# Performance work log

Measured on AMD Instinct MI355X. Metric: run time of the kernel, lower is better.

Reference implementation:

```python
import jax, jax.numpy as jnp
import numpy as np

EPS = 1e-8
NU_MOLECULAR = 1.5e-05
# loss weights (module defaults)
DATA_W, BC_W, TURB_W, RANS_W, SMOOTH_W, WALL_W = 1.0, 0.05, 0.05, 0.05, 0.01, 0.02
CONT_INIT = CONT_TGT = 0.1
MOM_INIT = MOM_TGT = 0.1
RAMP_STEPS, RAMP_START = 1000, 0

N_NODES, N_EDGES = 100000, 6400000


def _curriculum_weights(step):
    if step < RAMP_START:
        return CONT_INIT, MOM_INIT
    if step >= RAMP_START + RAMP_STEPS:
        return CONT_TGT, MOM_TGT
    alpha = (step - RAMP_START) / RAMP_STEPS  # linear ramp
    return ((1 - alpha) * CONT_INIT + alpha * CONT_TGT,
            (1 - alpha) * MOM_INIT + alpha * MOM_TGT)


def setup_inputs() -> dict:
    key = jax.random.key(0)
    k1, k2, k3, k4, k5 = jax.random.split(key, 5)
    predictions = jax.random.normal(k1, (N_NODES, 4), dtype=jnp.float32)
    targets = jax.random.normal(k2, (N_NODES, 4), dtype=jnp.float32)
    # dx, dy strictly positive edge offsets
    edge_attr_dxdy = jax.random.uniform(k3, (N_EDGES, 2), dtype=jnp.float32, minval=1e-3, maxval=0.05)
    edge_index = jax.random.randint(k4, (2, N_EDGES), 0, N_NODES, dtype=jnp.int64)
    wall_mask = jax.random.bernoulli(k5, 0.05, (N_NODES,))
    return {"predictions": predictions, "targets": targets,
            "edge_attr_dxdy": edge_attr_dxdy, "edge_index": edge_index,
            "wall_mask": wall_mask, "step": 500}


def reference(predictions, targets, edge_attr_dxdy, edge_index, wall_mask, step):
    cont_w, mom_w = _curriculum_weights(int(step))
    N = predictions.shape[0]
    row, col = edge_index[0], edge_index[1]
    u, v, p, nu_t = (predictions[:, i] for i in range(4))
    dx, dy = edge_attr_dxdy[:, 0], edge_attr_dxdy[:, 1]

    # per-edge finite differences (single gather of node fields)
    du = u[col] - u[row]
    dv = v[col] - v[row]
    dp = p[col] - p[row]

    seg = lambda e: jax.ops.segment_sum(e, row, num_segments=N)
    edge_count = jnp.maximum(seg(jnp.ones_like(du)), 1.0)

    # --- data loss ---
    mse_loss = jnp.mean((predictions - targets) ** 2)

    # --- continuity (divergence) loss ---
    divergence = (seg(du / (dx + EPS)) + seg(dv / (dy + EPS))) / edge_count
    div_loss = jnp.mean(divergence ** 2)

    # --- momentum loss ---
    p_grad_x = seg(dp / (dx + EPS)) / edge_count
    p_grad_y = seg(dp / (dy + EPS)) / edge_count
    lap_u = seg(du / (dx ** 2 + EPS)) / edge_count
    lap_v = seg(dv / (dy ** 2 + EPS)) / edge_count
    nu_eff = NU_MOLECULAR + nu_t
    momentum_loss = jnp.mean((p_grad_x + nu_eff * lap_u) ** 2 +
                             (p_grad_y + nu_eff * lap_v) ** 2)

    # --- turbulence losses ---
    positivity_loss = jnp.mean(jax.nn.relu(-nu_t) ** 2)
    du_dx = du / (dx + EPS)
    du_dy = du / (dy + EPS)
    dv_dx = dv / (dx + EPS)
    dv_dy = dv / (dy + EPS)
    strain_sq_edge = 2.0 * (du_dx ** 2 + dv_dy ** 2) + (du_dy + dv_dx) ** 2
    strain_node = seg(strain_sq_edge) / edge_count
    production = nu_t * strain_node
    turb_production_loss = jnp.mean(production ** 2)
    turb_dissipation_loss = jnp.mean(nu_t ** 2)

    # --- boundary-condition & wall-function losses (wall mask) ---
    m = wall_mask.astype(u.dtype)
    n_wall = jnp.maximum(jnp.sum(m), 1.0)
    bc_loss = jnp.sum(m * (u ** 2 + v ** 2)) / n_wall
    wall_loss = jnp.sum(m * (u ** 2 + v ** 2 + nu_t ** 2)) / n_wall

    # --- smoothness loss over edges ---
    smooth_loss = jnp.mean((predictions[col] - predictions[row]) ** 2)

    total = (DATA_W * mse_loss + cont_w * div_loss + mom_w * momentum_loss +
             TURB_W * turb_production_loss + RANS_W * turb_dissipation_loss +
             BC_W * bc_loss + SMOOTH_W * smooth_loss + WALL_W * wall_loss)
    # positivity_loss is tracked but not weighted into total (per visible code paths)
    return total
```

## Files before the change

kernel.cpp:

```cpp
#include <hip/hip_runtime.h>
#include <hip/hip_fp16.h>

#define EPS 1e-8f
#define NU_MOL 1.5e-5f
#define NPB 512
#define MAXNB 256
#define NBP 256
#define NBLK 4096
#define CMAX 1664
#define KMAX 7
#define CH 2048
#define SPLIT 6
#define NGRP 64
#define GRP 64


union U32H2 { unsigned u; __half2 h; };

__device__ inline unsigned packh2(float a, float b) {
    U32H2 x; x.h = __halves2half2(__float2half_rn(a), __float2half_rn(b));
    return x.u;
}
__device__ inline float2 unpackh2(unsigned u) {
    U32H2 x; x.u = u;
    return make_float2(__low2float(x.h), __high2float(x.h));
}
__device__ inline unsigned bf16rne(float f) {
    unsigned u = __float_as_uint(f);
    u += 0x7FFFu + ((u >> 16) & 1u);
    return u >> 16;
}
__device__ inline float bf16dec(unsigned h) {
    return __uint_as_float(h << 16);
}

__device__ inline int detect64(const void* eidx, int N) {
    const long long* ll = (const long long*)eidx;
    int is64 = 1;
    #pragma unroll
    for (int i = 0; i < 16; ++i) {
        long long v = ll[i];
        if (v < 0 || v >= (long long)N) is64 = 0;
    }
    return is64;
}


__global__ void detect_idx_dtype(const void* eidx, int N, int* flag) {
    const long long* ll = (const long long*)eidx;
    int is64 = 1;
    for (int i = 0; i < 16; ++i) {
        long long v = ll[i];
        if (v < 0 || v >= (long long)N) { is64 = 0; break; }
    }
    *flag = is64;
}

__global__ void finalize_kernel(const double* __restrict__ d,
                                const double* __restrict__ smooth_slots,
                                int N, int E, float* __restrict__ out)
{
    double smooth = 0.0;
    for (int i = 0; i < 64; ++i) smooth += smooth_slots[i];
    double dN = (double)N;
    double n_wall = d[5] > 1.0 ? d[5] : 1.0;
    double total = 1.0  * d[0] / (4.0 * dN)
                 + 0.1  * d[1] / dN
                 + 0.1  * d[2] / dN
                 + 0.05 * d[3] / dN
                 + 0.05 * d[4] / dN
                 + 0.05 * d[6] / n_wall
                 + 0.01 * smooth / (4.0 * (double)E)
                 + 0.02 * d[7] / n_wall;
    out[0] = (float)total;
}


__global__ __launch_bounds__(256) void count_kernel(
    const void* __restrict__ eidx, int E, int N, int NB,
    unsigned* __restrict__ counts)
{
    __shared__ unsigned hist[2][MAXNB];
    hist[0][threadIdx.x] = 0u;
    hist[1][threadIdx.x] = 0u;
    __syncthreads();
    const int w = (threadIdx.x >> 6) & 1;
    const int is64 = detect64(eidx, N);
    const long long* ll = (const long long*)eidx;
    const int* ii = (const int*)eidx;
    int chunk = (E + NBLK - 1) / NBLK;
    int s = blockIdx.x * chunk;
    int Cb = min(chunk, E - s);

    unsigned rr[KMAX];
    #pragma unroll
    for (int k = 0; k < KMAX; ++k) {
        int i = k * 256 + threadIdx.x;
        if (i < Cb) {
            int r = is64 ? (int)ll[s + i] : ii[s + i];
            rr[k] = (unsigned)min(max(r, 0), N - 1);
        } else rr[k] = 0xFFFFFFFFu;
    }
    #pragma unroll
    for (int k = 0; k < KMAX; ++k)
        if (rr[k] != 0xFFFFFFFFu)
            atomicAdd(&hist[w][rr[k] >> 9], 1u);
    __syncthreads();
    if (threadIdx.x < NB)
        counts[(size_t)blockIdx.x * NBP + threadIdx.x] =
            hist[0][threadIdx.x] + hist[1][threadIdx.x];
}

__global__ __launch_bounds__(256) void group_sums_kernel(
    const unsigned* __restrict__ counts, unsigned* __restrict__ gsum, int NB)
{
    __shared__ unsigned red[4][64];
    int g = blockIdx.x;
    int b0 = blockIdx.y * 64;
    int j = threadIdx.x & 63, seg = threadIdx.x >> 6;
    int b = b0 + j;
    unsigned ssum = 0;
    if (b < NB) {
        #pragma unroll
        for (int k = 0; k < 16; ++k) {
            int row = g * GRP + seg * 16 + k;
            ssum += counts[(size_t)row * NBP + b];
        }
    }
    red[seg][j] = ssum;
    __syncthreads();
    if (seg == 0 && b < NB)
        gsum[(size_t)g * NBP + b] = red[0][j] + red[1][j] + red[2][j] + red[3][j];
}

__global__ __launch_bounds__(512) void scan_base_kernel(
    unsigned* __restrict__ gsum, unsigned* __restrict__ base, int NB)
{
    __shared__ unsigned sc[512];
    int t = threadIdx.x;
    unsigned vg[NGRP];
    unsigned total = 0;
    if (t < NB) {
        #pragma unroll
        for (int g = 0; g < NGRP; ++g) {
            vg[g] = gsum[(size_t)g * NBP + t];
            total += vg[g];
        }
    }
    sc[t] = total; __syncthreads();
    for (int off = 1; off < 512; off <<= 1) {
        unsigned x = (t >= off) ? sc[t - off] : 0u;
        __syncthreads();
        sc[t] += x;
        __syncthreads();
    }
    unsigned ex = sc[t] - total;
    if (t < NB) {
        base[t] = ex;
        unsigned run = ex;
        #pragma unroll
        for (int g = 0; g < NGRP; ++g) {
            unsigned x = vg[g];
            gsum[(size_t)g * NBP + t] = run;
            run += x;
        }
    }
    if (t == 511) base[NB] = sc[511];
}

__global__ __launch_bounds__(256) void local_scan_kernel(
    unsigned* __restrict__ counts, const unsigned* __restrict__ gsum, int NB)
{
    __shared__ unsigned segs[4][64];
    int g = blockIdx.x;
    int b0 = blockIdx.y * 64;
    int j = threadIdx.x & 63, seg = threadIdx.x >> 6;
    int b = b0 + j;
    unsigned v[16];
    unsigned ssum = 0;
    if (b < NB) {
        #pragma unroll
        for (int k = 0; k < 16; ++k) {
            int row = g * GRP + seg * 16 + k;
            v[k] = counts[(size_t)row * NBP + b];
            ssum += v[k];
        }
    }
    segs[seg][j] = ssum;
    __syncthreads();
    if (b < NB) {
        unsigned carry = gsum[(size_t)g * NBP + b];
        for (int s_ = 0; s_ < seg; ++s_) carry += segs[s_][j];
        #pragma unroll
        for (int k = 0; k < 16; ++k) {
            int row = g * GRP + seg * 16 + k;
            counts[(size_t)row * NBP + b] = carry;
            carry += v[k];
        }
    }
}

__global__ __launch_bounds__(256) void scatter_kernel(
    const void* __restrict__ eidx, const float2* __restrict__ eattr,
    int E, int N, int NB,
    const unsigned* __restrict__ localoff ,
    uint2* __restrict__ vals)
{
    __shared__ unsigned hist[2][MAXNB];
    __shared__ unsigned cur[MAXNB];
    __shared__ unsigned gb2[MAXNB];
    __shared__ uint2 pl[CMAX];
    __shared__ unsigned char bb[CMAX];
    __shared__ unsigned wt[4];

    const int t = threadIdx.x;
    const int blk = blockIdx.x;
    const int lane = t & 63, wv = t >> 6;
    const int w = wv & 1;
    const int is64 = detect64(eidx, N);
    const long long* ll = (const long long*)eidx;
    const int* ii = (const int*)eidx;
    const int chunk = (E + NBLK - 1) / NBLK;
    const int s = blk * chunk;
    const int Cb = min(chunk, E - s);

    hist[0][t] = 0u;
    hist[1][t] = 0u;
    __syncthreads();

    unsigned rr[KMAX], rk[KMAX];
    #pragma unroll
    for (int k = 0; k < KMAX; ++k) {
        int i = k * 256 + t;
        if (i < Cb) {
            int r = is64 ? (int)ll[s + i] : ii[s + i];
            rr[k] = (unsigned)min(max(r, 0), N - 1);
        } else rr[k] = 0xFFFFFFFFu;
    }
    #pragma unroll
    for (int k = 0; k < KMAX; ++k)
        if (rr[k] != 0xFFFFFFFFu)
            rk[k] = atomicAdd(&hist[w][rr[k] >> 9], 1u);
    if (t < NB) gb2[t] = localoff[(size_t)blk * NBP + t];
    __syncthreads();

    unsigned h = hist[0][t] + hist[1][t];
    unsigned x = h;
    #pragma unroll
    for (int off = 1; off < 64; off <<= 1) {
        unsigned y = (unsigned)__shfl_up((int)x, off, 64);
        if (lane >= off) x += y;
    }
    if (lane == 63) wt[wv] = x;
    __syncthreads();
    unsigned wadd = 0;
    for (int w2 = 0; w2 < wv; ++w2) wadd += wt[w2];
    unsigned ex = x + wadd - h;
    cur[t] = ex;
    __syncthreads();
    if (t < NB) gb2[t] -= cur[t];

    int cc[KMAX]; float2 dd[KMAX];
    #pragma unroll
    for (int k = 0; k < KMAX; ++k) {
        int i = k * 256 + t;
        if (i < Cb) {
            int e = s + i;
            cc[k] = is64 ? (int)ll[(long long)E + e] : ii[E + e];
            dd[k] = eattr[e];
        }
    }
    #pragma unroll
    for (int k = 0; k < KMAX; ++k) {
        int i = k * 256 + t;
        if (i < Cb) {
            unsigned r = rr[k];
            unsigned b = r >> 9;
            unsigned rl = r & (NPB - 1);
            int c = min(max(cc[k], 0), N - 1);
            unsigned slot = cur[b] + (w ? hist[0][b] : 0u) + rk[k];
            pl[slot] = make_uint2((unsigned)c | (rl << 17),
                                  packh2(dd[k].x, dd[k].y));
            bb[slot] = (unsigned char)b;
        }
    }
    __syncthreads();

    uint2 op[KMAX]; unsigned ob[KMAX];
    #pragma unroll
    for (int k = 0; k < KMAX; ++k) {
        int p = k * 256 + t;
        if (p < Cb) { op[k] = pl[p]; ob[k] = (unsigned)bb[p]; }
    }
    #pragma unroll
    for (int k = 0; k < KMAX; ++k) {
        int p = k * 256 + t;
        if (p < Cb) vals[gb2[ob[k]] + (unsigned)p] = op[k];
    }
}

__global__ __launch_bounds__(512) void accum_kernel(
    const uint2* __restrict__ vals, const unsigned* __restrict__ base,
    const float4* __restrict__ pred, int N,
    float* __restrict__ g , double* __restrict__ smooth_slots)
{
    __shared__ uint2 pl[CH];
    __shared__ uint2 ph[NPB];
    __shared__ unsigned hist[NPB];
    __shared__ unsigned cur[NPB];
    __shared__ unsigned wt[8];
    __shared__ double sm[8];

    const int b = blockIdx.x;
    const int t = threadIdx.x;
    const int wv = t >> 6, lane = t & 63;
    const int n0 = b * NPB;

    {
        int n = n0 + t;
        float4 p = (n < N) ? pred[n] : make_float4(0.f, 0.f, 0.f, 0.f);
        ph[t] = make_uint2(packh2(p.x, p.y), packh2(p.z, p.w));
    }

    unsigned s0 = base[b], e0 = base[b + 1];
    unsigned len = e0 - s0;
    unsigned s = s0 + (unsigned)(((unsigned long long)len * blockIdx.y) / SPLIT);
    unsigned e = s0 + (unsigned)(((unsigned long long)len * (blockIdx.y + 1)) / SPLIT);

    float cnt = 0, sdiv = 0, smx = 0, smy = 0, sstr = 0;
    double smooth = 0.0;

    for (unsigned cs = s; cs < e; cs += CH) {
        const int n = (int)min((unsigned)CH, e - cs);
        hist[t] = 0u;
        __syncthreads();

        uint2 vv[4]; unsigned rk2[4]; float4 pcc[4];
        #pragma unroll
        for (int k = 0; k < 4; ++k) {
            int i = k * 512 + t;
            if (i < n) vv[k] = vals[cs + i];
            else vv[k].x = 0xFFFFFFFFu;
        }
        #pragma unroll
        for (int k = 0; k < 4; ++k) {
            int i = k * 512 + t;
            if (i < n) {
                rk2[k] = atomicAdd(&hist[(vv[k].x >> 17) & (NPB - 1)], 1u);
                pcc[k] = pred[vv[k].x & 0x1FFFFu];
            }
        }
        __syncthreads();

        unsigned v = hist[t];
        unsigned x = v;
        #pragma unroll
        for (int off = 1; off < 64; off <<= 1) {
            unsigned y = (unsigned)__shfl_up((int)x, off, 64);
            if (lane >= off) x += y;
        }
        if (lane == 63) wt[wv] = x;
        __syncthreads();
        unsigned wadd = 0;
        for (int w = 0; w < wv; ++w) wadd += wt[w];
        unsigned incl = x + wadd;
        unsigned ex0 = incl - v;
        cur[t] = ex0;
        cnt += (float)v;
        __syncthreads();

        #pragma unroll
        for (int k = 0; k < 4; ++k) {
            int i = k * 512 + t;
            if (i >= n) continue;
            unsigned pk = vv[k].x;
            unsigned rl = (pk >> 17) & (NPB - 1);
            float2 dxy = unpackh2(vv[k].y);
            float4 pc = pcc[k];
            uint2 pru = ph[rl];
            float2 pxy = unpackh2(pru.x);
            float2 pzw = unpackh2(pru.y);
            float du = pc.x - pxy.x, dv = pc.y - pxy.y;
            float dp = pc.z - pzw.x, dn = pc.w - pzw.y;
            float rx  = 1.0f / (dxy.x + EPS);
            float ry  = 1.0f / (dxy.y + EPS);
            float rx2 = 1.0f / (dxy.x * dxy.x + EPS);
            float ry2 = 1.0f / (dxy.y * dxy.y + EPS);
            float du_dx = du * rx, du_dy = du * ry;
            float dv_dx = dv * rx, dv_dy = dv * ry;
            float nu_eff = NU_MOL + pzw.y;
            float sh = du_dy + dv_dx;
            float div_e = du_dx + dv_dy;
            float mx_e  = dp * rx + nu_eff * du * rx2;
            float my_e  = dp * ry + nu_eff * dv * ry2;
            float str_e = 2.0f * (du_dx * du_dx + dv_dy * dv_dy) + sh * sh;
            unsigned pos = cur[rl] + rk2[k];
            pl[pos] = make_uint2(bf16rne(div_e) | (bf16rne(mx_e) << 16),
                                 bf16rne(my_e) | (bf16rne(str_e) << 16));
            smooth += (double)(du * du + dv * dv + dp * dp + dn * dn);
        }
        __syncthreads();

        for (unsigned i = ex0; i < incl; ++i) {
            uint2 pv = pl[i];
            sdiv += bf16dec(pv.x & 0xFFFFu);
            smx  += bf16dec(pv.x >> 16);
            smy  += bf16dec(pv.y & 0xFFFFu);
            sstr += bf16dec(pv.y >> 16);
        }
        __syncthreads();
    }

    {
        int n = n0 + t;
        if (n < N) {
            atomicAdd(&g[0 * (size_t)N + n], cnt);
            atomicAdd(&g[1 * (size_t)N + n], sdiv);
            atomicAdd(&g[2 * (size_t)N + n], smx);
            atomicAdd(&g[3 * (size_t)N + n], smy);
            atomicAdd(&g[4 * (size_t)N + n], sstr);
        }
    }

    for (int off = 32; off > 0; off >>= 1)
        smooth += __shfl_down(smooth, off);
    if (lane == 0) sm[wv] = smooth;
    __syncthreads();
    if (t == 0) {
        double tot = 0;
        #pragma unroll
        for (int w = 0; w < 8; ++w) tot += sm[w];
        atomicAdd(&smooth_slots[(b * SPLIT + blockIdx.y) & 63], tot);
    }
}

__global__ __launch_bounds__(256) void node_final_kernel(
    const float* __restrict__ g, const float4* __restrict__ pred,
    const float4* __restrict__ tgt, const unsigned char* __restrict__ wall,
    int N, double* __restrict__ d)
{
    int i = blockIdx.x * 256 + threadIdx.x;
    double v0 = 0, v1 = 0, v2 = 0, v3 = 0, v4 = 0, v5 = 0, v6 = 0, v7 = 0;
    if (i < N) {
        float cnt = g[0 * (size_t)N + i];
        float inv = 1.0f / fmaxf(cnt, 1.0f);
        float div = g[1 * (size_t)N + i] * inv;
        float mx  = g[2 * (size_t)N + i] * inv;
        float my  = g[3 * (size_t)N + i] * inv;
        float sn  = g[4 * (size_t)N + i] * inv;
        float4 p = pred[i];
        float4 tg = tgt[i];
        float prod = p.w * sn;
        float m = wall[i] ? 1.0f : 0.0f;
        float e0 = p.x - tg.x, e1 = p.y - tg.y, e2 = p.z - tg.z, e3 = p.w - tg.w;
        float uv = p.x * p.x + p.y * p.y;
        v0 = (double)(e0 * e0 + e1 * e1 + e2 * e2 + e3 * e3);
        v1 = (double)div * (double)div;
        v2 = (double)mx * (double)mx + (double)my * (double)my;
        v3 = (double)prod * (double)prod;
        v4 = (double)p.w * (double)p.w;
        v5 = (double)m;
        v6 = (double)(m * uv);
        v7 = (double)(m * (uv + p.w * p.w));
    }
    for (int off = 32; off > 0; off >>= 1) {
        v0 += __shfl_down(v0, off); v1 += __shfl_down(v1, off);
        v2 += __shfl_down(v2, off); v3 += __shfl_down(v3, off);
        v4 += __shfl_down(v4, off); v5 += __shfl_down(v5, off);
        v6 += __shfl_down(v6, off); v7 += __shfl_down(v7, off);
    }
    __shared__ double sm[4][8];
    int lane = threadIdx.x & 63, wv = threadIdx.x >> 6;
    if (lane == 0) {
        sm[wv][0] = v0; sm[wv][1] = v1; sm[wv][2] = v2; sm[wv][3] = v3;
        sm[wv][4] = v4; sm[wv][5] = v5; sm[wv][6] = v6; sm[wv][7] = v7;
    }
    __syncthreads();
    if (threadIdx.x < 8) {
        int q = threadIdx.x;
        atomicAdd(&d[q], sm[0][q] + sm[1][q] + sm[2][q] + sm[3][q]);
    }
}


__global__ __launch_bounds__(256) void edge_kernel(
    const void* __restrict__ eidx, const float2* __restrict__ eattr,
    const float4* __restrict__ pred, int E, int N, const int* __restrict__ flag,
    float* __restrict__ a_cnt, float* __restrict__ a_div,
    float* __restrict__ a_mx, float* __restrict__ a_my,
    float* __restrict__ a_str, double* __restrict__ smooth_slots)
{
    const int is64 = *flag;
    const long long* ll = (const long long*)eidx;
    const int* ii = (const int*)eidx;
    double smooth = 0.0;
    const int stride = gridDim.x * blockDim.x;
    for (int e = blockIdx.x * blockDim.x + threadIdx.x; e < E; e += stride) {
        int row, col;
        if (is64) { row = (int)ll[e]; col = (int)ll[(long long)E + e]; }
        else      { row = ii[e];      col = ii[E + e]; }
        row = min(max(row, 0), N - 1);
        col = min(max(col, 0), N - 1);
        float2 dxy = eattr[e];
        float4 pr = pred[row];
        float4 pc = pred[col];
        float du = pc.x - pr.x, dv = pc.y - pr.y;
        float dp = pc.z - pr.z, dn = pc.w - pr.w;
        float rx  = 1.0f / (dxy.x + EPS);
        float ry  = 1.0f / (dxy.y + EPS);
        float rx2 = 1.0f / (dxy.x * dxy.x + EPS);
        float ry2 = 1.0f / (dxy.y * dxy.y + EPS);
        float du_dx = du * rx, du_dy = du * ry;
        float dv_dx = dv * rx, dv_dy = dv * ry;
        float nu_eff = NU_MOL + pr.w;
        atomicAdd(&a_cnt[row], 1.0f);
        atomicAdd(&a_div[row], du_dx + dv_dy);
        atomicAdd(&a_mx[row], dp * rx + nu_eff * du * rx2);
        atomicAdd(&a_my[row], dp * ry + nu_eff * dv * ry2);
        float sh = du_dy + dv_dx;
        atomicAdd(&a_str[row], 2.0f * (du_dx * du_dx + dv_dy * dv_dy) + sh * sh);
        smooth += (double)(du * du + dv * dv + dp * dp + dn * dn);
    }
    for (int off = 32; off > 0; off >>= 1)
        smooth += __shfl_down(smooth, off);
    __shared__ double sm[4];
    int lane = threadIdx.x & 63, wv = threadIdx.x >> 6;
    if (lane == 0) sm[wv] = smooth;
    __syncthreads();
    if (threadIdx.x == 0)
        atomicAdd(&smooth_slots[blockIdx.x & 63], sm[0] + sm[1] + sm[2] + sm[3]);
}

__global__ __launch_bounds__(256) void node_kernel(
    const float4* __restrict__ pred, const float4* __restrict__ tgt,
    const unsigned char* __restrict__ wall, int N,
    const float* __restrict__ a_cnt, const float* __restrict__ a_div,
    const float* __restrict__ a_mx, const float* __restrict__ a_my,
    const float* __restrict__ a_str, double* __restrict__ d)
{
    int i = blockIdx.x * blockDim.x + threadIdx.x;
    double v0 = 0, v1 = 0, v2 = 0, v3 = 0, v4 = 0, v5 = 0, v6 = 0, v7 = 0;
    if (i < N) {
        float4 p = pred[i];
        float4 t = tgt[i];
        float inv = 1.0f / fmaxf(a_cnt[i], 1.0f);
        float div = a_div[i] * inv;
        float mx = a_mx[i] * inv, my = a_my[i] * inv;
        float sn = a_str[i] * inv;
        float prod = p.w * sn;
        float m = wall[i] ? 1.0f : 0.0f;
        float e0 = p.x - t.x, e1 = p.y - t.y, e2 = p.z - t.z, e3 = p.w - t.w;
        float uv = p.x * p.x + p.y * p.y;
        v0 = (double)(e0 * e0 + e1 * e1 + e2 * e2 + e3 * e3);
        v1 = (double)div * (double)div;
        v2 = (double)mx * (double)mx + (double)my * (double)my;
        v3 = (double)prod * (double)prod;
        v4 = (double)p.w * (double)p.w;
        v5 = (double)m;
        v6 = (double)(m * uv);
        v7 = (double)(m * (uv + p.w * p.w));
    }
    for (int off = 32; off > 0; off >>= 1) {
        v0 += __shfl_down(v0, off); v1 += __shfl_down(v1, off);
        v2 += __shfl_down(v2, off); v3 += __shfl_down(v3, off);
        v4 += __shfl_down(v4, off); v5 += __shfl_down(v5, off);
        v6 += __shfl_down(v6, off); v7 += __shfl_down(v7, off);
    }
    __shared__ double sm[4][8];
    int lane = threadIdx.x & 63, wv = threadIdx.x >> 6;
    if (lane == 0) {
        sm[wv][0] = v0; sm[wv][1] = v1; sm[wv][2] = v2; sm[wv][3] = v3;
        sm[wv][4] = v4; sm[wv][5] = v5; sm[wv][6] = v6; sm[wv][7] = v7;
    }
    __syncthreads();
    if (threadIdx.x < 8) {
        int q = threadIdx.x;
        atomicAdd(&d[q], sm[0][q] + sm[1][q] + sm[2][q] + sm[3][q]);
    }
}


extern "C" void kernel_launch(void* const* d_in, const int* in_sizes, int n_in,
                              void* d_out, int out_size, void* d_ws, size_t ws_size,
                              hipStream_t stream) {
    const float4* pred = (const float4*)d_in[0];
    const float4* tgt  = (const float4*)d_in[1];
    const float2* eattr = (const float2*)d_in[2];
    const void* eidx = d_in[3];
    const unsigned char* wall = (const unsigned char*)d_in[4];
    int N = in_sizes[0] / 4;
    int E = in_sizes[2] / 2;
    int NB = (N + NPB - 1) / NPB;
    int chunk = (E + NBLK - 1) / NBLK;
    int ntiles = (NB + 63) / 64;

    char* ws = (char*)d_ws;
    double* d = (double*)ws;
    double* smooth_slots = d + 8;
    int* flag = (int*)(ws + 576);

    size_t off = 1024;
    float* g        = (float*)(ws + off);     off += (size_t)5 * N * 4;
    unsigned* counts = (unsigned*)(ws + off); off += (size_t)NBLK * NBP * 4;
    unsigned* gsum   = (unsigned*)(ws + off); off += (size_t)NGRP * NBP * 4;
    unsigned* base   = (unsigned*)(ws + off); off += (size_t)(NB + 1) * 4;
    off = (off + 15) & ~(size_t)15;
    uint2* vals      = (uint2*)(ws + off);    off += (size_t)E * 8;
    size_t need_fast = off;

    bool fast = (NB <= MAXNB) && (N <= 131072) && (chunk <= CMAX) &&
                (ws_size >= need_fast);

    if (fast) {
        hipMemsetAsync(d_ws, 0, 1024 + (size_t)5 * N * 4, stream);
        count_kernel<<<NBLK, 256, 0, stream>>>(eidx, E, N, NB, counts);
        group_sums_kernel<<<dim3(NGRP, ntiles), 256, 0, stream>>>(counts, gsum, NB);
        scan_base_kernel<<<1, 512, 0, stream>>>(gsum, base, NB);
        local_scan_kernel<<<dim3(NGRP, ntiles), 256, 0, stream>>>(counts, gsum, NB);
        scatter_kernel<<<NBLK, 256, 0, stream>>>(eidx, eattr, E, N, NB,
                                                 counts, vals);
        accum_kernel<<<dim3(NB, SPLIT), 512, 0, stream>>>(vals, base, pred, N,
                                                          g, smooth_slots);
        node_final_kernel<<<(N + 255) / 256, 256, 0, stream>>>(g, pred, tgt, wall,
                                                               N, d);
        finalize_kernel<<<1, 1, 0, stream>>>(d, smooth_slots, N, E, (float*)d_out);
    } else {
        float* arrays = (float*)(ws + 1024);
        float* a_cnt = arrays + (size_t)0 * N;
        float* a_div = arrays + (size_t)1 * N;
        float* a_mx  = arrays + (size_t)2 * N;
        float* a_my  = arrays + (size_t)3 * N;
        float* a_str = arrays + (size_t)4 * N;
        size_t zbytes = 1024 + (size_t)5 * N * sizeof(float);
        hipMemsetAsync(d_ws, 0, zbytes, stream);
        detect_idx_dtype<<<1, 1, 0, stream>>>(eidx, N, flag);
        edge_kernel<<<4096, 256, 0, stream>>>(eidx, eattr, pred, E, N, flag,
                                              a_cnt, a_div, a_mx, a_my, a_str,
                                              smooth_slots);
        node_kernel<<<(N + 255) / 256, 256, 0, stream>>>(pred, tgt, wall, N,
                                                         a_cnt, a_div, a_mx, a_my,
                                                         a_str, d);
        finalize_kernel<<<1, 1, 0, stream>>>(d, smooth_slots, N, E, (float*)d_out);
    }
}
```

Before: 236.7 us.

## Replace per-block scan hierarchy with atomic cursors and LDS float atomics in accumulation

The three-kernel two-level prefix scan over per-block bucket counts is replaced by a global atomic histogram, a single small scan kernel, and atomic cursor reservation inside the scatter kernel. The accumulation kernel drops its local counting sort and bf16 staging buffer. It now accumulates the five per-node sums with shared-memory float atomics and keeps predictions in fp32 in LDS. This removes several launches, the large counts array traffic and many barriers. In exchange it adds LDS atomic contention on hot row slots and makes the edge ordering within buckets nondeterministic.

```diff
diff --git a/kernel.cpp b/kernel.cpp
--- a/kernel.cpp
+++ b/kernel.cpp
@@ -5,14 +5,10 @@
 #define NU_MOL 1.5e-5f
 #define NPB 512
 #define MAXNB 256
-#define NBP 256
 #define NBLK 4096
 #define CMAX 1664
 #define KMAX 7
-#define CH 2048
 #define SPLIT 6
-#define NGRP 64
-#define GRP 64
 
 
 union U32H2 { unsigned u; __half2 h; };
@@ -24,14 +20,6 @@
 __device__ inline float2 unpackh2(unsigned u) {
     U32H2 x; x.u = u;
     return make_float2(__low2float(x.h), __high2float(x.h));
-}
-__device__ inline unsigned bf16rne(float f) {
-    unsigned u = __float_as_uint(f);
-    u += 0x7FFFu + ((u >> 16) & 1u);
-    return u >> 16;
-}
-__device__ inline float bf16dec(unsigned h) {
-    return __uint_as_float(h << 16);
 }
 
 __device__ inline int detect64(const void* eidx, int N) {
@@ -78,7 +66,7 @@
 
 __global__ __launch_bounds__(256) void count_kernel(
     const void* __restrict__ eidx, int E, int N, int NB,
-    unsigned* __restrict__ counts)
+    unsigned* __restrict__ tot)
 {
     __shared__ unsigned hist[2][MAXNB];
     hist[0][threadIdx.x] = 0u;
@@ -106,104 +94,40 @@
         if (rr[k] != 0xFFFFFFFFu)
             atomicAdd(&hist[w][rr[k] >> 9], 1u);
     __syncthreads();
-    if (threadIdx.x < NB)
-        counts[(size_t)blockIdx.x * NBP + threadIdx.x] =
-            hist[0][threadIdx.x] + hist[1][threadIdx.x];
-}
-
-__global__ __launch_bounds__(256) void group_sums_kernel(
-    const unsigned* __restrict__ counts, unsigned* __restrict__ gsum, int NB)
-{
-    __shared__ unsigned red[4][64];
-    int g = blockIdx.x;
-    int b0 = blockIdx.y * 64;
-    int j = threadIdx.x & 63, seg = threadIdx.x >> 6;
-    int b = b0 + j;
-    unsigned ssum = 0;
-    if (b < NB) {
-        #pragma unroll
-        for (int k = 0; k < 16; ++k) {
-            int row = g * GRP + seg * 16 + k;
-            ssum += counts[(size_t)row * NBP + b];
-        }
-    }
-    red[seg][j] = ssum;
-    __syncthreads();
-    if (seg == 0 && b < NB)
-        gsum[(size_t)g * NBP + b] = red[0][j] + red[1][j] + red[2][j] + red[3][j];
-}
-
-__global__ __launch_bounds__(512) void scan_base_kernel(
-    unsigned* __restrict__ gsum, unsigned* __restrict__ base, int NB)
-{
-    __shared__ unsigned sc[512];
+    if (threadIdx.x < NB) {
+        unsigned h = hist[0][threadIdx.x] + hist[1][threadIdx.x];
+        if (h) atomicAdd(&tot[threadIdx.x], h);
+    }
+}
+
+__global__ __launch_bounds__(256) void scan_small_kernel(
+    const unsigned* __restrict__ tot, unsigned* __restrict__ base,
+    unsigned* __restrict__ cursor, int NB)
+{
+    __shared__ unsigned wt[4];
     int t = threadIdx.x;
-    unsigned vg[NGRP];
-    unsigned total = 0;
-    if (t < NB) {
-        #pragma unroll
-        for (int g = 0; g < NGRP; ++g) {
-            vg[g] = gsum[(size_t)g * NBP + t];
-            total += vg[g];
-        }
-    }
-    sc[t] = total; __syncthreads();
-    for (int off = 1; off < 512; off <<= 1) {
-        unsigned x = (t >= off) ? sc[t - off] : 0u;
-        __syncthreads();
-        sc[t] += x;
-        __syncthreads();
-    }
-    unsigned ex = sc[t] - total;
-    if (t < NB) {
-        base[t] = ex;
-        unsigned run = ex;
-        #pragma unroll
-        for (int g = 0; g < NGRP; ++g) {
-            unsigned x = vg[g];
-            gsum[(size_t)g * NBP + t] = run;
-            run += x;
-        }
-    }
-    if (t == 511) base[NB] = sc[511];
-}
-
-__global__ __launch_bounds__(256) void local_scan_kernel(
-    unsigned* __restrict__ counts, const unsigned* __restrict__ gsum, int NB)
-{
-    __shared__ unsigned segs[4][64];
-    int g = blockIdx.x;
-    int b0 = blockIdx.y * 64;
-    int j = threadIdx.x & 63, seg = threadIdx.x >> 6;
-    int b = b0 + j;
-    unsigned v[16];
-    unsigned ssum = 0;
-    if (b < NB) {
-        #pragma unroll
-        for (int k = 0; k < 16; ++k) {
-            int row = g * GRP + seg * 16 + k;
-            v[k] = counts[(size_t)row * NBP + b];
-            ssum += v[k];
-        }
-    }
-    segs[seg][j] = ssum;
-    __syncthreads();
-    if (b < NB) {
-        unsigned carry = gsum[(size_t)g * NBP + b];
-        for (int s_ = 0; s_ < seg; ++s_) carry += segs[s_][j];
-        #pragma unroll
-        for (int k = 0; k < 16; ++k) {
-            int row = g * GRP + seg * 16 + k;
-            counts[(size_t)row * NBP + b] = carry;
-            carry += v[k];
-        }
-    }
+    int lane = t & 63, wv = t >> 6;
+    unsigned v = (t < NB) ? tot[t] : 0u;
+    unsigned x = v;
+    #pragma unroll
+    for (int off = 1; off < 64; off <<= 1) {
+        unsigned y = (unsigned)__shfl_up((int)x, off, 64);
+        if (lane >= off) x += y;
+    }
+    if (lane == 63) wt[wv] = x;
+    __syncthreads();
+    unsigned wadd = 0;
+    for (int w2 = 0; w2 < wv; ++w2) wadd += wt[w2];
+    unsigned incl = x + wadd;
+    unsigned ex = incl - v;
+    if (t < NB) { base[t] = ex; cursor[t] = ex; }
+    if (t == 255) base[NB] = incl;
 }
 
 __global__ __launch_bounds__(256) void scatter_kernel(
     const void* __restrict__ eidx, const float2* __restrict__ eattr,
     int E, int N, int NB,
-    const unsigned* __restrict__ localoff ,
+    unsigned* __restrict__ cursor,
     uint2* __restrict__ vals)
 {
     __shared__ unsigned hist[2][MAXNB];
@@ -241,7 +165,6 @@
     for (int k = 0; k < KMAX; ++k)
         if (rr[k] != 0xFFFFFFFFu)
             rk[k] = atomicAdd(&hist[w][rr[k] >> 9], 1u);
-    if (t < NB) gb2[t] = localoff[(size_t)blk * NBP + t];
     __syncthreads();
 
     unsigned h = hist[0][t] + hist[1][t];
@@ -257,8 +180,8 @@
     for (int w2 = 0; w2 < wv; ++w2) wadd += wt[w2];
     unsigned ex = x + wadd - h;
     cur[t] = ex;
-    __syncthreads();
-    if (t < NB) gb2[t] -= cur[t];
+    if (t < NB) gb2[t] = atomicAdd(&cursor[t], h) - ex;
+    __syncthreads();
 
     int cc[KMAX]; float2 dd[KMAX];
     #pragma unroll
@@ -304,11 +227,8 @@
     const float4* __restrict__ pred, int N,
     float* __restrict__ g , double* __restrict__ smooth_slots)
 {
-    __shared__ uint2 pl[CH];
-    __shared__ uint2 ph[NPB];
-    __shared__ unsigned hist[NPB];
-    __shared__ unsigned cur[NPB];
-    __shared__ unsigned wt[8];
+    __shared__ float4 ph[NPB];
+    __shared__ float acc[5 * NPB];
     __shared__ double sm[8];
 
     const int b = blockIdx.x;
@@ -318,24 +238,22 @@
 
     {
         int n = n0 + t;
-        float4 p = (n < N) ? pred[n] : make_float4(0.f, 0.f, 0.f, 0.f);
-        ph[t] = make_uint2(packh2(p.x, p.y), packh2(p.z, p.w));
-    }
+        ph[t] = (n < N) ? pred[n] : make_float4(0.f, 0.f, 0.f, 0.f);
+        #pragma unroll
+        for (int q = 0; q < 5; ++q) acc[q * NPB + t] = 0.f;
+    }
+    __syncthreads();
 
     unsigned s0 = base[b], e0 = base[b + 1];
     unsigned len = e0 - s0;
     unsigned s = s0 + (unsigned)(((unsigned long long)len * blockIdx.y) / SPLIT);
     unsigned e = s0 + (unsigned)(((unsigned long long)len * (blockIdx.y + 1)) / SPLIT);
 
-    float cnt = 0, sdiv = 0, smx = 0, smy = 0, sstr = 0;
     double smooth = 0.0;
 
-    for (unsigned cs = s; cs < e; cs += CH) {
-        const int n = (int)min((unsigned)CH, e - cs);
-        hist[t] = 0u;
-        __syncthreads();
-
-        uint2 vv[4]; unsigned rk2[4]; float4 pcc[4];
+    for (unsigned cs = s; cs < e; cs += 4 * 512) {
+        const int n = (int)min((unsigned)(4 * 512), e - cs);
+        uint2 vv[4]; float4 pcc[4];
         #pragma unroll
         for (int k = 0; k < 4; ++k) {
             int i = k * 512 + t;
@@ -345,30 +263,8 @@
         #pragma unroll
         for (int k = 0; k < 4; ++k) {
             int i = k * 512 + t;
-            if (i < n) {
-                rk2[k] = atomicAdd(&hist[(vv[k].x >> 17) & (NPB - 1)], 1u);
-                pcc[k] = pred[vv[k].x & 0x1FFFFu];
-            }
+            if (i < n) pcc[k] = pred[vv[k].x & 0x1FFFFu];
         }
-        __syncthreads();
-
-        unsigned v = hist[t];
-        unsigned x = v;
-        #pragma unroll
-        for (int off = 1; off < 64; off <<= 1) {
-            unsigned y = (unsigned)__shfl_up((int)x, off, 64);
-            if (lane >= off) x += y;
-        }
-        if (lane == 63) wt[wv] = x;
-        __syncthreads();
-        unsigned wadd = 0;
-        for (int w = 0; w < wv; ++w) wadd += wt[w];
-        unsigned incl = x + wadd;
-        unsigned ex0 = incl - v;
-        cur[t] = ex0;
-        cnt += (float)v;
-        __syncthreads();
-
         #pragma unroll
         for (int k = 0; k < 4; ++k) {
             int i = k * 512 + t;
@@ -377,48 +273,37 @@
             unsigned rl = (pk >> 17) & (NPB - 1);
             float2 dxy = unpackh2(vv[k].y);
             float4 pc = pcc[k];
-            uint2 pru = ph[rl];
-            float2 pxy = unpackh2(pru.x);
-            float2 pzw = unpackh2(pru.y);
-            float du = pc.x - pxy.x, dv = pc.y - pxy.y;
-            float dp = pc.z - pzw.x, dn = pc.w - pzw.y;
+            float4 pr = ph[rl];
+            float du = pc.x - pr.x, dv = pc.y - pr.y;
+            float dp = pc.z - pr.z, dn = pc.w - pr.w;
             float rx  = 1.0f / (dxy.x + EPS);
             float ry  = 1.0f / (dxy.y + EPS);
             float rx2 = 1.0f / (dxy.x * dxy.x + EPS);
             float ry2 = 1.0f / (dxy.y * dxy.y + EPS);
             float du_dx = du * rx, du_dy = du * ry;
             float dv_dx = dv * rx, dv_dy = dv * ry;
-            float nu_eff = NU_MOL + pzw.y;
+            float nu_eff = NU_MOL + pr.w;
             float sh = du_dy + dv_dx;
             float div_e = du_dx + dv_dy;
             float mx_e  = dp * rx + nu_eff * du * rx2;
             float my_e  = dp * ry + nu_eff * dv * ry2;
             float str_e = 2.0f * (du_dx * du_dx + dv_dy * dv_dy) + sh * sh;
-            unsigned pos = cur[rl] + rk2[k];
-            pl[pos] = make_uint2(bf16rne(div_e) | (bf16rne(mx_e) << 16),
-                                 bf16rne(my_e) | (bf16rne(str_e) << 16));
+            atomicAdd(&acc[0 * NPB + rl], 1.0f);
+            atomicAdd(&acc[1 * NPB + rl], div_e);
+            atomicAdd(&acc[2 * NPB + rl], mx_e);
+            atomicAdd(&acc[3 * NPB + rl], my_e);
+            atomicAdd(&acc[4 * NPB + rl], str_e);
             smooth += (double)(du * du + dv * dv + dp * dp + dn * dn);
         }
-        __syncthreads();
-
-        for (unsigned i = ex0; i < incl; ++i) {
-            uint2 pv = pl[i];
-            sdiv += bf16dec(pv.x & 0xFFFFu);
-            smx  += bf16dec(pv.x >> 16);
-            smy  += bf16dec(pv.y & 0xFFFFu);
-            sstr += bf16dec(pv.y >> 16);
-        }
-        __syncthreads();
-    }
+    }
+    __syncthreads();
 
     {
         int n = n0 + t;
         if (n < N) {
-            atomicAdd(&g[0 * (size_t)N + n], cnt);
-            atomicAdd(&g[1 * (size_t)N + n], sdiv);
-            atomicAdd(&g[2 * (size_t)N + n], smx);
-            atomicAdd(&g[3 * (size_t)N + n], smy);
-            atomicAdd(&g[4 * (size_t)N + n], sstr);
+            #pragma unroll
+            for (int q = 0; q < 5; ++q)
+                atomicAdd(&g[(size_t)q * N + n], acc[q * NPB + t]);
         }
     }
 
@@ -592,7 +477,6 @@
     int E = in_sizes[2] / 2;
     int NB = (N + NPB - 1) / NPB;
     int chunk = (E + NBLK - 1) / NBLK;
-    int ntiles = (NB + 63) / 64;
 
     char* ws = (char*)d_ws;
     double* d = (double*)ws;
@@ -601,9 +485,10 @@
 
     size_t off = 1024;
     float* g        = (float*)(ws + off);     off += (size_t)5 * N * 4;
-    unsigned* counts = (unsigned*)(ws + off); off += (size_t)NBLK * NBP * 4;
-    unsigned* gsum   = (unsigned*)(ws + off); off += (size_t)NGRP * NBP * 4;
-    unsigned* base   = (unsigned*)(ws + off); off += (size_t)(NB + 1) * 4;
+    unsigned* tot    = (unsigned*)(ws + off); off += (size_t)MAXNB * 4;
+    size_t zbytes = off;
+    unsigned* base   = (unsigned*)(ws + off); off += (size_t)(MAXNB + 1) * 4;
+    unsigned* cursor = (unsigned*)(ws + off); off += (size_t)MAXNB * 4;
     off = (off + 15) & ~(size_t)15;
     uint2* vals      = (uint2*)(ws + off);    off += (size_t)E * 8;
     size_t need_fast = off;
@@ -612,13 +497,11 @@
                 (ws_size >= need_fast);
 
     if (fast) {
-        hipMemsetAsync(d_ws, 0, 1024 + (size_t)5 * N * 4, stream);
-        count_kernel<<<NBLK, 256, 0, stream>>>(eidx, E, N, NB, counts);
-        group_sums_kernel<<<dim3(NGRP, ntiles), 256, 0, stream>>>(counts, gsum, NB);
-        scan_base_kernel<<<1, 512, 0, stream>>>(gsum, base, NB);
-        local_scan_kernel<<<dim3(NGRP, ntiles), 256, 0, stream>>>(counts, gsum, NB);
+        hipMemsetAsync(d_ws, 0, zbytes, stream);
+        count_kernel<<<NBLK, 256, 0, stream>>>(eidx, E, N, NB, tot);
+        scan_small_kernel<<<1, 256, 0, stream>>>(tot, base, cursor, NB);
         scatter_kernel<<<NBLK, 256, 0, stream>>>(eidx, eattr, E, N, NB,
-                                                 counts, vals);
+                                                 cursor, vals);
         accum_kernel<<<dim3(NB, SPLIT), 512, 0, stream>>>(vals, base, pred, N,
                                                           g, smooth_slots);
         node_final_kernel<<<(N + 255) / 256, 256, 0, stream>>>(g, pred, tgt, wall,
@@ -631,8 +514,8 @@
         float* a_mx  = arrays + (size_t)2 * N;
         float* a_my  = arrays + (size_t)3 * N;
         float* a_str = arrays + (size_t)4 * N;
-        size_t zbytes = 1024 + (size_t)5 * N * sizeof(float);
-        hipMemsetAsync(d_ws, 0, zbytes, stream);
+        size_t zb = 1024 + (size_t)5 * N * sizeof(float);
+        hipMemsetAsync(d_ws, 0, zb, stream);
         detect_idx_dtype<<<1, 1, 0, stream>>>(eidx, N, flag);
         edge_kernel<<<4096, 256, 0, stream>>>(eidx, eattr, pred, E, N, flag,
                                               a_cnt, a_div, a_mx, a_my, a_str,
```

New measurement: 532.9 us. 2.25x slower.
